# Kernel tuning notes

Measured on AMD Instinct MI355X. Metric: run time of the kernel, lower is better.

Reference implementation:

```python
import jax, jax.numpy as jnp
import numpy as np

SEQ, B, NP, NG = 100, 200, 512, 4096

def setup_inputs() -> dict:
    key = jax.random.key(0)
    ks = jax.random.split(key, 6)
    velocity = jax.random.normal(ks[0], (SEQ, B, 2), dtype=jnp.float32)
    init_pc = jax.random.uniform(ks[1], (B, NP), dtype=jnp.float32)
    # encoder: nn.Linear(Np, Ng, bias=False) -> weight (Ng, Np), default kaiming-uniform-ish; use uniform(+-1/sqrt(Np))
    lim_enc = 1.0 / np.sqrt(NP)
    W_enc = jax.random.uniform(ks[2], (NG, NP), minval=-lim_enc, maxval=lim_enc, dtype=jnp.float32)
    # RNN weights: weight_ih_l0 (Ng, 2), weight_hh_l0 (Ng, Ng); torch init uniform(+-1/sqrt(Ng))
    lim = 1.0 / np.sqrt(NG)
    W_ih = jax.random.uniform(ks[3], (NG, 2), minval=-lim, maxval=lim, dtype=jnp.float32)
    W_hh = jax.random.uniform(ks[4], (NG, NG), minval=-lim, maxval=lim, dtype=jnp.float32)
    # decoder: xavier_uniform on (Np, Ng)
    lim_dec = np.sqrt(6.0 / (NP + NG))
    W_dec = jax.random.uniform(ks[5], (NP, NG), minval=-lim_dec, maxval=lim_dec, dtype=jnp.float32)
    return {"velocity": velocity, "init_pc": init_pc, "W_enc": W_enc,
            "W_ih": W_ih, "W_hh": W_hh, "W_dec": W_dec}

def reference(velocity, init_pc, W_enc, W_ih, W_hh, W_dec):
    # h0 = encoder(init_pc): (B, Ng)
    h0 = init_pc @ W_enc.T
    # precompute input projections for all steps: (SEQ, B, Ng)
    vx = jnp.einsum('sbi,gi->sbg', velocity, W_ih)
    def step(h, v_t):
        h_new = jax.nn.relu(v_t + h @ W_hh.T)
        return h_new, h_new
    _, g = jax.lax.scan(step, h0, vx)          # g: (SEQ, B, Ng)
    place_logits = jnp.einsum('sbg,pg->sbp', g, W_dec)  # (SEQ, B, Np)
    return place_logits, g
```

## Files before the change

### kernel.cpp

```cpp
#include <hip/hip_runtime.h>
#include <cstdint>
#include <cstddef>

#define kSEQ 100
#define kB   200
#define kNP  512
#define kNG  4096
#define kMP  256
#define KSPLIT 8

typedef _Float16 f16_t;
typedef f16_t f16x8 __attribute__((ext_vector_type(8)));
typedef f16_t f16x4 __attribute__((ext_vector_type(4)));
typedef float f32x4 __attribute__((ext_vector_type(4)));

__device__ __forceinline__ void gld_lds16(const f16_t* g, f16_t* l) {
    __builtin_amdgcn_global_load_lds(
        (const __attribute__((address_space(1))) unsigned int*)g,
        (__attribute__((address_space(3))) unsigned int*)l, 16, 0, 0);
}

__global__ __launch_bounds__(256)
void k_half(const float* __restrict__ src, f16_t* __restrict__ dst, int n8) {
    int i = blockIdx.x * 256 + threadIdx.x;
    if (i >= n8) return;
    const float4* s = (const float4*)src + (size_t)i * 2;
    float4 v0 = s[0], v1 = s[1];
    f16x8 h;
    h[0] = (f16_t)v0.x; h[1] = (f16_t)v0.y; h[2] = (f16_t)v0.z; h[3] = (f16_t)v0.w;
    h[4] = (f16_t)v1.x; h[5] = (f16_t)v1.y; h[6] = (f16_t)v1.z; h[7] = (f16_t)v1.w;
    *(f16x8*)(dst + (size_t)i * 8) = h;
}

__global__ __launch_bounds__(512, 4)
void k_gemm_f16(const f16_t* __restrict__ A, int lda,
                const f16_t* __restrict__ B, int ldb,
                f16_t* __restrict__ part, int kPerChunk) {
    __shared__ __align__(16) f16_t sA[2][128 * 64];
    __shared__ __align__(16) f16_t sB[2][128 * 64];

    const int bid    = blockIdx.x;
    const int xcd    = bid & 7;
    const int idx    = bid >> 3;
    const int n_tile = xcd * 4 + (idx & 3);
    const int rem    = idx >> 2;
    const int kc     = rem >> 1;
    const int m_tile = rem & 1;

    const int tid  = threadIdx.x;
    const int lane = tid & 63;
    const int wid  = tid >> 6;
    const int wr   = wid >> 2;
    const int wc   = wid & 3;
    const int m0   = m_tile * 128;
    const int n0   = n_tile * 128;
    const int kBase = kc * kPerChunk;
    const int nIter = kPerChunk >> 6;

    f32x4 acc[4][2];
#pragma unroll
    for (int i = 0; i < 4; i++)
#pragma unroll
        for (int j = 0; j < 2; j++) acc[i][j] = (f32x4){0.f, 0.f, 0.f, 0.f};

    const int s0   = wid * 128 + lane;
    const int s1   = s0 + 64;
    const int r0s  = s0 >> 3, c0 = (s0 & 7) ^ (r0s & 7);
    const int r1s  = s1 >> 3, c1 = (s1 & 7) ^ (r1s & 7);
    const int b0   = (wid * 128) * 8;
    const int b1   = (wid * 128 + 64) * 8;

    const f16_t* gA0 = A + (size_t)(m0 + r0s) * (size_t)lda + c0 * 8;
    const f16_t* gA1 = A + (size_t)(m0 + r1s) * (size_t)lda + c1 * 8;
    const f16_t* gB0 = B + (size_t)(n0 + r0s) * (size_t)ldb + c0 * 8;
    const f16_t* gB1 = B + (size_t)(n0 + r1s) * (size_t)ldb + c1 * 8;

    gld_lds16(gA0 + kBase, &sA[0][b0]);
    gld_lds16(gA1 + kBase, &sA[0][b1]);
    gld_lds16(gB0 + kBase, &sB[0][b0]);
    gld_lds16(gB1 + kBase, &sB[0][b1]);
    __syncthreads();

    int cur = 0;
    for (int kb = 0; kb < nIter; ++kb) {
        if (kb + 1 < nIter) {
            const int kn = kBase + (kb + 1) * 64;
            gld_lds16(gA0 + kn, &sA[cur ^ 1][b0]);
            gld_lds16(gA1 + kn, &sA[cur ^ 1][b1]);
            gld_lds16(gB0 + kn, &sB[cur ^ 1][b0]);
            gld_lds16(gB1 + kn, &sB[cur ^ 1][b1]);
        }
        const f16_t* cA = sA[cur];
        const f16_t* cB = sB[cur];
#pragma unroll
        for (int ks2 = 0; ks2 < 2; ks2++) {
            f16x8 a[4], b[2];
            const unsigned int klane = (unsigned)(lane >> 4) * 16u + (unsigned)ks2 * 64u;
#pragma unroll
            for (int fm = 0; fm < 4; fm++) {
                const unsigned int row = (unsigned)(wr * 64 + fm * 16 + (lane & 15));
                const unsigned int off = (row * 128u + klane) ^ ((row & 7u) << 4);
                a[fm] = *(const f16x8*)((const char*)cA + off);
            }
#pragma unroll
            for (int fn = 0; fn < 2; fn++) {
                const unsigned int row = (unsigned)(wc * 32 + fn * 16 + (lane & 15));
                const unsigned int off = (row * 128u + klane) ^ ((row & 7u) << 4);
                b[fn] = *(const f16x8*)((const char*)cB + off);
            }
#pragma unroll
            for (int fm = 0; fm < 4; fm++)
#pragma unroll
                for (int fn = 0; fn < 2; fn++)
                    acc[fm][fn] = __builtin_amdgcn_mfma_f32_16x16x32_f16(a[fm], b[fn], acc[fm][fn], 0, 0, 0);
        }
        __syncthreads();
        cur ^= 1;
    }

    f16_t* po = part + (size_t)kc * ((size_t)kB * kNG);
#pragma unroll
    for (int fm = 0; fm < 4; fm++)
#pragma unroll
        for (int fn = 0; fn < 2; fn++) {
            const int row0 = m0 + wr * 64 + fm * 16 + ((lane >> 4) << 2);
            const int col  = n0 + wc * 32 + fn * 16 + (lane & 15);
#pragma unroll
            for (int j = 0; j < 4; j++) {
                const int row = row0 + j;
                if (row < kB)
                    po[(size_t)row * kNG + col] = (f16_t)acc[fm][fn][j];
            }
        }
}

__global__ __launch_bounds__(256)
void k_reduce(const f16_t* __restrict__ part,
              const float* __restrict__ velocity, const float* __restrict__ W_ih,
              float* __restrict__ gout, f16_t* __restrict__ gb,
              f16_t* __restrict__ hout, int t, int mode) {
    const int b = blockIdx.y;
    const int g = blockIdx.x * 1024 + threadIdx.x * 4;

    float v0 = 0.f, v1 = 0.f, v2 = 0.f, v3 = 0.f;
#pragma unroll
    for (int ks = 0; ks < KSPLIT; ks++) {
        f16x4 p = *(const f16x4*)(part + (size_t)ks * ((size_t)kB * kNG) + (size_t)b * kNG + g);
        v0 += (float)p[0]; v1 += (float)p[1]; v2 += (float)p[2]; v3 += (float)p[3];
    }
    if (mode == 1) {
        const float2 vel = *(const float2*)(velocity + ((size_t)t * kB + b) * 2);
        const float4 w01 = *(const float4*)(W_ih + (size_t)g * 2);
        const float4 w23 = *(const float4*)(W_ih + (size_t)g * 2 + 4);
        v0 = fmaxf(0.f, v0 + vel.x * w01.x + vel.y * w01.y);
        v1 = fmaxf(0.f, v1 + vel.x * w01.z + vel.y * w01.w);
        v2 = fmaxf(0.f, v2 + vel.x * w23.x + vel.y * w23.y);
        v3 = fmaxf(0.f, v3 + vel.x * w23.z + vel.y * w23.w);
        float4 o; o.x = v0; o.y = v1; o.z = v2; o.w = v3;
        *(float4*)(gout + ((size_t)t * kB + b) * kNG + g) = o;
    }
    f16x4 h;
    h[0] = (f16_t)v0; h[1] = (f16_t)v1; h[2] = (f16_t)v2; h[3] = (f16_t)v3;
    if (hout)
        *(f16x4*)(hout + (size_t)b * kNG + g) = h;
    if (mode == 1 && gb)
        *(f16x4*)(gb + ((size_t)t * kB + b) * kNG + g) = h;
}

__global__ __launch_bounds__(256)
void k_dec(const float* __restrict__ Gf, const f16_t* __restrict__ Gb,
           const f16_t* __restrict__ Wd, float* __restrict__ out) {
    __shared__ __align__(16) f16_t sA[128 * 64];
    __shared__ __align__(16) f16_t sB[128 * 64];

    const int bid  = blockIdx.x;
    const int xcd  = bid & 7;
    const int idx  = bid >> 3;
    const int tile = xcd * 79 + idx;
    if (tile >= 157 * 4) return;
    const int m0 = (tile >> 2) * 128;
    const int n0 = (tile & 3) * 128;

    const int tid  = threadIdx.x;
    const int lane = tid & 63;
    const int wid  = tid >> 6;
    const int wr   = wid >> 1;
    const int wc   = wid & 1;
    const int M    = kSEQ * kB;

    f32x4 acc[4][4];
#pragma unroll
    for (int i = 0; i < 4; i++)
#pragma unroll
        for (int j = 0; j < 4; j++) acc[i][j] = (f32x4){0.f, 0.f, 0.f, 0.f};

    const int sr   = tid >> 1;
    const int half = tid & 1;
    const int sc   = half * 32;
    const unsigned int swzrow = ((unsigned)sr & 7u) << 4;
    const unsigned int sbase  = (unsigned)sr * 128u + (unsigned)half * 64u;
    int arow = m0 + sr; if (arow > M - 1) arow = M - 1;

    for (int k0 = 0; k0 < kNG; k0 += 64) {
        __syncthreads();
        if (Gb) {
            const uint4* gA = (const uint4*)(Gb + (size_t)arow * kNG + k0 + sc);
#pragma unroll
            for (int i = 0; i < 4; i++) {
                unsigned int off = (sbase + (unsigned)i * 16u) ^ swzrow;
                *(uint4*)((char*)sA + off) = gA[i];
            }
        } else {
            const float4* gA = (const float4*)(Gf + (size_t)arow * kNG + k0 + sc);
#pragma unroll
            for (int i = 0; i < 4; i++) {
                float4 a0 = gA[2 * i], a1 = gA[2 * i + 1];
                f16x8 u;
                u[0] = (f16_t)a0.x; u[1] = (f16_t)a0.y; u[2] = (f16_t)a0.z; u[3] = (f16_t)a0.w;
                u[4] = (f16_t)a1.x; u[5] = (f16_t)a1.y; u[6] = (f16_t)a1.z; u[7] = (f16_t)a1.w;
                unsigned int off = (sbase + (unsigned)i * 16u) ^ swzrow;
                *(f16x8*)((char*)sA + off) = u;
            }
        }
        {
            const uint4* gB = (const uint4*)(Wd + (size_t)(n0 + sr) * kNG + k0 + sc);
#pragma unroll
            for (int i = 0; i < 4; i++) {
                unsigned int off = (sbase + (unsigned)i * 16u) ^ swzrow;
                *(uint4*)((char*)sB + off) = gB[i];
            }
        }
        __syncthreads();
#pragma unroll
        for (int ks2 = 0; ks2 < 2; ks2++) {
            f16x8 a[4], b[4];
            const unsigned int klane = (unsigned)(lane >> 4) * 16u + (unsigned)ks2 * 64u;
#pragma unroll
            for (int fm = 0; fm < 4; fm++) {
                const unsigned int row = (unsigned)(wr * 64 + fm * 16 + (lane & 15));
                const unsigned int off = (row * 128u + klane) ^ ((row & 7u) << 4);
                a[fm] = *(const f16x8*)((const char*)sA + off);
            }
#pragma unroll
            for (int fn = 0; fn < 4; fn++) {
                const unsigned int row = (unsigned)(wc * 64 + fn * 16 + (lane & 15));
                const unsigned int off = (row * 128u + klane) ^ ((row & 7u) << 4);
                b[fn] = *(const f16x8*)((const char*)sB + off);
            }
#pragma unroll
            for (int fm = 0; fm < 4; fm++)
#pragma unroll
                for (int fn = 0; fn < 4; fn++)
                    acc[fm][fn] = __builtin_amdgcn_mfma_f32_16x16x32_f16(a[fm], b[fn], acc[fm][fn], 0, 0, 0);
        }
    }

#pragma unroll
    for (int fm = 0; fm < 4; fm++)
#pragma unroll
        for (int fn = 0; fn < 4; fn++) {
            const int row0 = m0 + wr * 64 + fm * 16 + ((lane >> 4) << 2);
            const int col  = n0 + wc * 64 + fn * 16 + (lane & 15);
#pragma unroll
            for (int j = 0; j < 4; j++) {
                const int row = row0 + j;
                if (row < M) out[(size_t)row * kNP + col] = acc[fm][fn][j];
            }
        }
}

extern "C" void kernel_launch(void* const* d_in, const int* in_sizes, int n_in,
                              void* d_out, int out_size, void* d_ws, size_t ws_size,
                              hipStream_t stream) {
    const float* velocity = (const float*)d_in[0];
    const float* init_pc  = (const float*)d_in[1];
    const float* W_enc    = (const float*)d_in[2];
    const float* W_ih     = (const float*)d_in[3];
    const float* W_hh     = (const float*)d_in[4];
    const float* W_dec    = (const float*)d_in[5];

    float* logits = (float*)d_out;
    float* gout   = logits + (size_t)kSEQ * kB * kNP;

    char* ws = (char*)d_ws;
    size_t off = 0;
    auto alloc = [&](size_t bytes) -> void* {
        void* p = ws + off;
        off += (bytes + 255) & ~(size_t)255;
        return p;
    };
    f16_t* whh  = (f16_t*)alloc((size_t)kNG * kNG * 2);
    f16_t* wdec = (f16_t*)alloc((size_t)kNP * kNG * 2);
    f16_t* wenc = (f16_t*)alloc((size_t)kNG * kNP * 2);
    f16_t* ip   = (f16_t*)alloc((size_t)kMP * kNP * 2);
    f16_t* h_buf[2];
    h_buf[0] = (f16_t*)alloc((size_t)kMP * kNG * 2);
    h_buf[1] = (f16_t*)alloc((size_t)kMP * kNG * 2);
    f16_t* partial = (f16_t*)alloc((size_t)KSPLIT * kB * kNG * 2);
    f16_t* gb = nullptr;
    if (ws_size >= off + ((size_t)kSEQ * kB + kMP) * kNG * 2 + 4096)
        gb = (f16_t*)alloc(((size_t)kSEQ * kB + kMP) * kNG * 2);

    hipMemsetAsync(ip + (size_t)kB * kNP, 0, (size_t)(kMP - kB) * kNP * 2, stream);

    int n8;
    n8 = kNG * kNG / 8;
    k_half<<<(n8 + 255) / 256, 256, 0, stream>>>(W_hh, whh, n8);
    n8 = kNP * kNG / 8;
    k_half<<<(n8 + 255) / 256, 256, 0, stream>>>(W_dec, wdec, n8);
    n8 = kNG * kNP / 8;
    k_half<<<(n8 + 255) / 256, 256, 0, stream>>>(W_enc, wenc, n8);
    n8 = kB * kNP / 8;
    k_half<<<(n8 + 255) / 256, 256, 0, stream>>>(init_pc, ip, n8);

    dim3 gR(4, kB);

    k_gemm_f16<<<512, 512, 0, stream>>>(ip, kNP, wenc, kNP, partial, kNP / KSPLIT);
    k_reduce<<<gR, 256, 0, stream>>>(partial, velocity, W_ih, nullptr, nullptr, h_buf[0], 0, 0);

    if (gb) {
        const f16_t* Acur = h_buf[0];
        for (int t = 0; t < kSEQ; t++) {
            k_gemm_f16<<<512, 512, 0, stream>>>(Acur, kNG, whh, kNG, partial, kNG / KSPLIT);
            k_reduce<<<gR, 256, 0, stream>>>(partial, velocity, W_ih, gout, gb, nullptr, t, 1);
            Acur = gb + (size_t)t * kB * kNG;
        }
    } else {
        int p = 0;
        for (int t = 0; t < kSEQ; t++) {
            k_gemm_f16<<<512, 512, 0, stream>>>(h_buf[p], kNG, whh, kNG, partial, kNG / KSPLIT);
            k_reduce<<<gR, 256, 0, stream>>>(partial, velocity, W_ih, gout, nullptr, h_buf[p ^ 1], t, 1);
            p ^= 1;
        }
    }

    k_dec<<<632, 256, 0, stream>>>(gout, gb, wdec, logits);
}
```

Baseline: 2.074 ms.

## Merge both M tiles into one 1024-thread block sharing each B tile

The recurrent GEMM kernel now uses 256 blocks of 1024 threads covering the full 256-row M extent, instead of 512 blocks of 512 threads each covering half of M. Each W_hh (B) tile is loaded into LDS once and shared by both M halves, which halves global/L2 traffic for the large weight matrix at every step. The costs are fewer, larger blocks, a larger LDS footprint (96 KB) that limits blocks per CU, and fewer loads in flight per thread.

Result: slower. 2.342 ms (+12.9%).

```diff
diff --git a/kernel.cpp b/kernel.cpp
--- a/kernel.cpp
+++ b/kernel.cpp
@@ -32,27 +32,24 @@
     *(f16x8*)(dst + (size_t)i * 8) = h;
 }
 
-__global__ __launch_bounds__(512, 4)
+__global__ __launch_bounds__(1024, 4)
 void k_gemm_f16(const f16_t* __restrict__ A, int lda,
                 const f16_t* __restrict__ B, int ldb,
                 f16_t* __restrict__ part, int kPerChunk) {
-    __shared__ __align__(16) f16_t sA[2][128 * 64];
+    __shared__ __align__(16) f16_t sA[2][256 * 64];
     __shared__ __align__(16) f16_t sB[2][128 * 64];
 
     const int bid    = blockIdx.x;
     const int xcd    = bid & 7;
     const int idx    = bid >> 3;
     const int n_tile = xcd * 4 + (idx & 3);
-    const int rem    = idx >> 2;
-    const int kc     = rem >> 1;
-    const int m_tile = rem & 1;
+    const int kc     = idx >> 2;
 
     const int tid  = threadIdx.x;
     const int lane = tid & 63;
     const int wid  = tid >> 6;
     const int wr   = wid >> 2;
     const int wc   = wid & 3;
-    const int m0   = m_tile * 128;
     const int n0   = n_tile * 128;
     const int kBase = kc * kPerChunk;
     const int nIter = kPerChunk >> 6;
@@ -63,32 +60,30 @@
 #pragma unroll
         for (int j = 0; j < 2; j++) acc[i][j] = (f32x4){0.f, 0.f, 0.f, 0.f};
 
-    const int s0   = wid * 128 + lane;
-    const int s1   = s0 + 64;
-    const int r0s  = s0 >> 3, c0 = (s0 & 7) ^ (r0s & 7);
-    const int r1s  = s1 >> 3, c1 = (s1 & 7) ^ (r1s & 7);
-    const int b0   = (wid * 128) * 8;
-    const int b1   = (wid * 128 + 64) * 8;
-
-    const f16_t* gA0 = A + (size_t)(m0 + r0s) * (size_t)lda + c0 * 8;
-    const f16_t* gA1 = A + (size_t)(m0 + r1s) * (size_t)lda + c1 * 8;
-    const f16_t* gB0 = B + (size_t)(n0 + r0s) * (size_t)ldb + c0 * 8;
-    const f16_t* gB1 = B + (size_t)(n0 + r1s) * (size_t)ldb + c1 * 8;
-
-    gld_lds16(gA0 + kBase, &sA[0][b0]);
-    gld_lds16(gA1 + kBase, &sA[0][b1]);
-    gld_lds16(gB0 + kBase, &sB[0][b0]);
-    gld_lds16(gB1 + kBase, &sB[0][b1]);
+    const int sa0 = wid * 64 + lane;
+    const int sa1 = sa0 + 1024;
+    const int ra0 = sa0 >> 3, ca0 = (sa0 & 7) ^ (ra0 & 7);
+    const int ra1 = sa1 >> 3, ca1 = (sa1 & 7) ^ (ra1 & 7);
+    const int rb0 = sa0 >> 3, cb0 = ca0;
+    const int ba0 = sa0 * 8, ba1 = sa1 * 8;
+    const int bb0 = sa0 * 8;
+
+    const f16_t* gA0 = A + (size_t)ra0 * (size_t)lda + ca0 * 8;
+    const f16_t* gA1 = A + (size_t)ra1 * (size_t)lda + ca1 * 8;
+    const f16_t* gB0 = B + (size_t)(n0 + rb0) * (size_t)ldb + cb0 * 8;
+
+    gld_lds16(gA0 + kBase, &sA[0][ba0]);
+    gld_lds16(gA1 + kBase, &sA[0][ba1]);
+    gld_lds16(gB0 + kBase, &sB[0][bb0]);
     __syncthreads();
 
     int cur = 0;
     for (int kb = 0; kb < nIter; ++kb) {
         if (kb + 1 < nIter) {
             const int kn = kBase + (kb + 1) * 64;
-            gld_lds16(gA0 + kn, &sA[cur ^ 1][b0]);
-            gld_lds16(gA1 + kn, &sA[cur ^ 1][b1]);
-            gld_lds16(gB0 + kn, &sB[cur ^ 1][b0]);
-            gld_lds16(gB1 + kn, &sB[cur ^ 1][b1]);
+            gld_lds16(gA0 + kn, &sA[cur ^ 1][ba0]);
+            gld_lds16(gA1 + kn, &sA[cur ^ 1][ba1]);
+            gld_lds16(gB0 + kn, &sB[cur ^ 1][bb0]);
         }
         const f16_t* cA = sA[cur];
         const f16_t* cB = sB[cur];
@@ -123,7 +118,7 @@
     for (int fm = 0; fm < 4; fm++)
 #pragma unroll
         for (int fn = 0; fn < 2; fn++) {
-            const int row0 = m0 + wr * 64 + fm * 16 + ((lane >> 4) << 2);
+            const int row0 = wr * 64 + fm * 16 + ((lane >> 4) << 2);
             const int col  = n0 + wc * 32 + fn * 16 + (lane & 15);
 #pragma unroll
             for (int j = 0; j < 4; j++) {
@@ -315,20 +310,20 @@
 
     dim3 gR(4, kB);
 
-    k_gemm_f16<<<512, 512, 0, stream>>>(ip, kNP, wenc, kNP, partial, kNP / KSPLIT);
+    k_gemm_f16<<<256, 1024, 0, stream>>>(ip, kNP, wenc, kNP, partial, kNP / KSPLIT);
     k_reduce<<<gR, 256, 0, stream>>>(partial, velocity, W_ih, nullptr, nullptr, h_buf[0], 0, 0);
 
     if (gb) {
         const f16_t* Acur = h_buf[0];
         for (int t = 0; t < kSEQ; t++) {
-            k_gemm_f16<<<512, 512, 0, stream>>>(Acur, kNG, whh, kNG, partial, kNG / KSPLIT);
+            k_gemm_f16<<<256, 1024, 0, stream>>>(Acur, kNG, whh, kNG, partial, kNG / KSPLIT);
             k_reduce<<<gR, 256, 0, stream>>>(partial, velocity, W_ih, gout, gb, nullptr, t, 1);
             Acur = gb + (size_t)t * kB * kNG;
         }
     } else {
         int p = 0;
         for (int t = 0; t < kSEQ; t++) {
-            k_gemm_f16<<<512, 512, 0, stream>>>(h_buf[p], kNG, whh, kNG, partial, kNG / KSPLIT);
+            k_gemm_f16<<<256, 1024, 0, stream>>>(h_buf[p], kNG, whh, kNG, partial, kNG / KSPLIT);
             k_reduce<<<gR, 256, 0, stream>>>(partial, velocity, W_ih, gout, nullptr, h_buf[p ^ 1], t, 1);
             p ^= 1;
         }
```

## Skip padded-row MFMAs in recurrent GEMM and widen decoder blocks to 8 waves

Applied to the files above, without the earlier changes.

In the recurrent k_gemm_f16 kernel, waves that cover only padding rows past batch 200 (second M tile, lower half) now load a single A fragment and issue MFMAs for one 16-row slice instead of four. This cuts wasted matrix work on the critical per-step path. Separately, the decoder GEMM moves from 256 to 512 threads per block with a 2x4 wave grid, so each wave holds fewer accumulators and the LDS staging work is spread over more threads. The tradeoff is possible wave divergence in the recurrent kernel and more threads synchronizing per decoder block.

Result: slower. 2.163 ms (+4.3%).

```diff
diff --git a/kernel.cpp b/kernel.cpp
--- a/kernel.cpp
+++ b/kernel.cpp
@@ -57,6 +57,8 @@
     const int kBase = kc * kPerChunk;
     const int nIter = kPerChunk >> 6;
 
+    const int fmax = (m_tile == 1 && wr == 1) ? 1 : 4;
+
     f32x4 acc[4][2];
 #pragma unroll
     for (int i = 0; i < 4; i++)
@@ -98,9 +100,11 @@
             const unsigned int klane = (unsigned)(lane >> 4) * 16u + (unsigned)ks2 * 64u;
 #pragma unroll
             for (int fm = 0; fm < 4; fm++) {
-                const unsigned int row = (unsigned)(wr * 64 + fm * 16 + (lane & 15));
-                const unsigned int off = (row * 128u + klane) ^ ((row & 7u) << 4);
-                a[fm] = *(const f16x8*)((const char*)cA + off);
+                if (fm < fmax) {
+                    const unsigned int row = (unsigned)(wr * 64 + fm * 16 + (lane & 15));
+                    const unsigned int off = (row * 128u + klane) ^ ((row & 7u) << 4);
+                    a[fm] = *(const f16x8*)((const char*)cA + off);
+                }
             }
 #pragma unroll
             for (int fn = 0; fn < 2; fn++) {
@@ -109,10 +113,13 @@
                 b[fn] = *(const f16x8*)((const char*)cB + off);
             }
 #pragma unroll
-            for (int fm = 0; fm < 4; fm++)
-#pragma unroll
-                for (int fn = 0; fn < 2; fn++)
-                    acc[fm][fn] = __builtin_amdgcn_mfma_f32_16x16x32_f16(a[fm], b[fn], acc[fm][fn], 0, 0, 0);
+            for (int fm = 0; fm < 4; fm++) {
+                if (fm < fmax) {
+#pragma unroll
+                    for (int fn = 0; fn < 2; fn++)
+                        acc[fm][fn] = __builtin_amdgcn_mfma_f32_16x16x32_f16(a[fm], b[fn], acc[fm][fn], 0, 0, 0);
+                }
+            }
         }
         __syncthreads();
         cur ^= 1;
@@ -167,7 +174,7 @@
         *(f16x4*)(gb + ((size_t)t * kB + b) * kNG + g) = h;
 }
 
-__global__ __launch_bounds__(256)
+__global__ __launch_bounds__(512)
 void k_dec(const float* __restrict__ Gf, const f16_t* __restrict__ Gb,
            const f16_t* __restrict__ Wd, float* __restrict__ out) {
     __shared__ __align__(16) f16_t sA[128 * 64];
@@ -184,56 +191,48 @@
     const int tid  = threadIdx.x;
     const int lane = tid & 63;
     const int wid  = tid >> 6;
-    const int wr   = wid >> 1;
-    const int wc   = wid & 1;
+    const int wr   = wid >> 2;
+    const int wc   = wid & 3;
     const int M    = kSEQ * kB;
 
-    f32x4 acc[4][4];
+    f32x4 acc[4][2];
 #pragma unroll
     for (int i = 0; i < 4; i++)
 #pragma unroll
-        for (int j = 0; j < 4; j++) acc[i][j] = (f32x4){0.f, 0.f, 0.f, 0.f};
-
-    const int sr   = tid >> 1;
-    const int half = tid & 1;
-    const int sc   = half * 32;
-    const unsigned int swzrow = ((unsigned)sr & 7u) << 4;
-    const unsigned int sbase  = (unsigned)sr * 128u + (unsigned)half * 64u;
-    int arow = m0 + sr; if (arow > M - 1) arow = M - 1;
+        for (int j = 0; j < 2; j++) acc[i][j] = (f32x4){0.f, 0.f, 0.f, 0.f};
+
+    const int c0  = tid, c1 = tid + 512;
+    const int r0  = c0 >> 3, k0c = c0 & 7;
+    const int r1  = c1 >> 3, k1c = c1 & 7;
+    const unsigned int off0 = ((unsigned)r0 * 128u + (unsigned)k0c * 16u) ^ (((unsigned)r0 & 7u) << 4);
+    const unsigned int off1 = ((unsigned)r1 * 128u + (unsigned)k1c * 16u) ^ (((unsigned)r1 & 7u) << 4);
+    int arow0 = m0 + r0; if (arow0 > M - 1) arow0 = M - 1;
+    int arow1 = m0 + r1; if (arow1 > M - 1) arow1 = M - 1;
 
     for (int k0 = 0; k0 < kNG; k0 += 64) {
         __syncthreads();
         if (Gb) {
-            const uint4* gA = (const uint4*)(Gb + (size_t)arow * kNG + k0 + sc);
-#pragma unroll
-            for (int i = 0; i < 4; i++) {
-                unsigned int off = (sbase + (unsigned)i * 16u) ^ swzrow;
-                *(uint4*)((char*)sA + off) = gA[i];
-            }
+            *(uint4*)((char*)sA + off0) = *(const uint4*)(Gb + (size_t)arow0 * kNG + k0 + k0c * 8);
+            *(uint4*)((char*)sA + off1) = *(const uint4*)(Gb + (size_t)arow1 * kNG + k0 + k1c * 8);
         } else {
-            const float4* gA = (const float4*)(Gf + (size_t)arow * kNG + k0 + sc);
-#pragma unroll
-            for (int i = 0; i < 4; i++) {
-                float4 a0 = gA[2 * i], a1 = gA[2 * i + 1];
-                f16x8 u;
-                u[0] = (f16_t)a0.x; u[1] = (f16_t)a0.y; u[2] = (f16_t)a0.z; u[3] = (f16_t)a0.w;
-                u[4] = (f16_t)a1.x; u[5] = (f16_t)a1.y; u[6] = (f16_t)a1.z; u[7] = (f16_t)a1.w;
-                unsigned int off = (sbase + (unsigned)i * 16u) ^ swzrow;
-                *(f16x8*)((char*)sA + off) = u;
-            }
-        }
-        {
-            const uint4* gB = (const uint4*)(Wd + (size_t)(n0 + sr) * kNG + k0 + sc);
-#pragma unroll
-            for (int i = 0; i < 4; i++) {
-                unsigned int off = (sbase + (unsigned)i * 16u) ^ swzrow;
-                *(uint4*)((char*)sB + off) = gB[i];
-            }
-        }
+            const float4* gA0 = (const float4*)(Gf + (size_t)arow0 * kNG + k0 + k0c * 8);
+            const float4* gA1 = (const float4*)(Gf + (size_t)arow1 * kNG + k0 + k1c * 8);
+            float4 a0 = gA0[0], a1 = gA0[1];
+            f16x8 u;
+            u[0] = (f16_t)a0.x; u[1] = (f16_t)a0.y; u[2] = (f16_t)a0.z; u[3] = (f16_t)a0.w;
+            u[4] = (f16_t)a1.x; u[5] = (f16_t)a1.y; u[6] = (f16_t)a1.z; u[7] = (f16_t)a1.w;
+            *(f16x8*)((char*)sA + off0) = u;
+            a0 = gA1[0]; a1 = gA1[1];
+            u[0] = (f16_t)a0.x; u[1] = (f16_t)a0.y; u[2] = (f16_t)a0.z; u[3] = (f16_t)a0.w;
+            u[4] = (f16_t)a1.x; u[5] = (f16_t)a1.y; u[6] = (f16_t)a1.z; u[7] = (f16_t)a1.w;
+            *(f16x8*)((char*)sA + off1) = u;
+        }
+        *(uint4*)((char*)sB + off0) = *(const uint4*)(Wd + (size_t)(n0 + r0) * kNG + k0 + k0c * 8);
+        *(uint4*)((char*)sB + off1) = *(const uint4*)(Wd + (size_t)(n0 + r1) * kNG + k0 + k1c * 8);
         __syncthreads();
 #pragma unroll
         for (int ks2 = 0; ks2 < 2; ks2++) {
-            f16x8 a[4], b[4];
+            f16x8 a[4], b[2];
             const unsigned int klane = (unsigned)(lane >> 4) * 16u + (unsigned)ks2 * 64u;
 #pragma unroll
             for (int fm = 0; fm < 4; fm++) {
@@ -242,15 +241,15 @@
                 a[fm] = *(const f16x8*)((const char*)sA + off);
             }
 #pragma unroll
-            for (int fn = 0; fn < 4; fn++) {
-                const unsigned int row = (unsigned)(wc * 64 + fn * 16 + (lane & 15));
+            for (int fn = 0; fn < 2; fn++) {
+                const unsigned int row = (unsigned)(wc * 32 + fn * 16 + (lane & 15));
                 const unsigned int off = (row * 128u + klane) ^ ((row & 7u) << 4);
                 b[fn] = *(const f16x8*)((const char*)sB + off);
             }
 #pragma unroll
             for (int fm = 0; fm < 4; fm++)
 #pragma unroll
-                for (int fn = 0; fn < 4; fn++)
+                for (int fn = 0; fn < 2; fn++)
                     acc[fm][fn] = __builtin_amdgcn_mfma_f32_16x16x32_f16(a[fm], b[fn], acc[fm][fn], 0, 0, 0);
         }
     }
@@ -258,9 +257,9 @@
 #pragma unroll
     for (int fm = 0; fm < 4; fm++)
 #pragma unroll
-        for (int fn = 0; fn < 4; fn++) {
+        for (int fn = 0; fn < 2; fn++) {
             const int row0 = m0 + wr * 64 + fm * 16 + ((lane >> 4) << 2);
-            const int col  = n0 + wc * 64 + fn * 16 + (lane & 15);
+            const int col  = n0 + wc * 32 + fn * 16 + (lane & 15);
 #pragma unroll
             for (int j = 0; j < 4; j++) {
                 const int row = row0 + j;
@@ -334,5 +333,5 @@
         }
     }
 
-    k_dec<<<632, 256, 0, stream>>>(gout, gb, wdec, logits);
-}
+    k_dec<<<632, 512, 0, stream>>>(gout, gb, wdec, logits);
+}
```
